# Performance work log

Hardware: AMD Instinct MI355X
Metric: run time of the kernel (lower is better)

## Reference

```python
import jax, jax.numpy as jnp
import numpy as np

B, D, W, T = 1024, 128, 512, 8
MAX_STEPS = 48
RTOL, ATOL = 1e-3, 1e-6
SAFETY, FMIN, FMAX = 0.9, 0.2, 10.0

# Tsit5 (Tsitouras 5(4)) tableau
A21 = 0.161
A31, A32 = -0.008480655492356989, 0.335480655492357
A41, A42, A43 = 2.8971530571054935, -6.359448489975075, 4.3622954328695815
A51, A52, A53, A54 = 5.325864828439257, -11.748883564062828, 7.4955393428898365, -0.09249506636175525
A61, A62, A63, A64, A65 = 5.86145544294642, -12.92096931784711, 8.159367898576159, -0.071584973281401, -0.028269050394068383
B1, B2, B3, B4, B5, B6 = 0.09646076681806523, 0.01, 0.4798896504144996, 1.379008574103742, -3.290069515436081, 2.324710524099774
E1, E2, E3, E4, E5, E6, E7 = (-0.00178001105222577714, -0.0008164344596567469, 0.007880878010261995,
                              -0.1447110071732629, 0.5823571654525552, -0.45808210592918697,
                              0.015151515151515152)


def setup_inputs() -> dict:
    key = jax.random.key(0)
    ks = jax.random.split(key, 9)
    def lin(k, fan_in, fan_out):
        s = 1.0 / np.sqrt(fan_in)
        return jax.random.normal(k, (fan_out, fan_in), jnp.float32) * s
    ts = jnp.linspace(0.0, 1.0, T, dtype=jnp.float32)
    y0 = jax.random.normal(ks[0], (B, D), jnp.float32)
    return {
        "ts": ts, "y0": y0,
        "W0": lin(ks[1], D, W), "b0": jnp.zeros((W,), jnp.float32),
        "W1": lin(ks[2], W, W), "b1": jnp.zeros((W,), jnp.float32),
        "W2": lin(ks[3], W, D), "b2": jnp.zeros((D,), jnp.float32),
    }


def _solve(ts, y0, W0, b0, W1, b1, W2, b2):
    def f(y):  # MLP vector field: D -> W -> W -> D, softplus activations
        h = jax.nn.softplus(y @ W0.T + b0)
        h = jax.nn.softplus(h @ W1.T + b1)
        return h @ W2.T + b2

    nT = ts.shape[0]
    ys0 = jnp.zeros((nT,) + y0.shape, y0.dtype).at[0].set(y0)  # SaveAt includes t0
    carry0 = (ts[0], ts[1] - ts[0], y0, jnp.int32(1), ys0)

    def step(carry, _):
        t, dt, y, si, ys = carry
        done = si >= nT
        si_c = jnp.minimum(si, nT - 1)
        tns = ts[si_c]
        # clip step to next save time (one shared dt across batch: unvmap_dt=True)
        h = jnp.where(done, 0.0, jnp.maximum(jnp.minimum(dt, tns - t), 0.0))
        k1 = f(y)
        k2 = f(y + h * (A21 * k1))
        k3 = f(y + h * (A31 * k1 + A32 * k2))
        k4 = f(y + h * (A41 * k1 + A42 * k2 + A43 * k3))
        k5 = f(y + h * (A51 * k1 + A52 * k2 + A53 * k3 + A54 * k4))
        k6 = f(y + h * (A61 * k1 + A62 * k2 + A63 * k3 + A64 * k4 + A65 * k5))
        y_new = y + h * (B1 * k1 + B2 * k2 + B3 * k3 + B4 * k4 + B5 * k5 + B6 * k6)
        k7 = f(y_new)
        err = h * (E1 * k1 + E2 * k2 + E3 * k3 + E4 * k4 + E5 * k5 + E6 * k6 + E7 * k7)
        scale = ATOL + RTOL * jnp.maximum(jnp.abs(y), jnp.abs(y_new))
        enorm = jnp.sqrt(jnp.mean((err / scale) ** 2))  # global norm -> shared dt
        accept = (enorm <= 1.0) & (~done)
        t_new = t + h
        hit = accept & (t_new >= tns - 1e-6)
        y = jnp.where(accept, y_new, y)
        t = jnp.where(accept, t_new, t)
        cur = jax.lax.dynamic_index_in_dim(ys, si_c, 0, keepdims=False)
        ys = jax.lax.dynamic_update_index_in_dim(ys, jnp.where(hit, y, cur), si_c, 0)
        si = si + hit.astype(si.dtype)
        safe_e = jnp.where(enorm > 0.0, enorm, 1.0)
        factor = jnp.where(enorm > 0.0, jnp.clip(SAFETY * safe_e ** (-0.2), FMIN, FMAX), FMAX)
        dt = jnp.where(done, dt, dt * factor)
        return (t, dt, y, si, ys), None

    (_, _, _, _, ys), _ = jax.lax.scan(step, carry0, None, length=MAX_STEPS)
    return ys  # [T, B, D]


def reference(ts, y0, W0, b0, W1, b1, W2, b2):
    return _solve(ts, y0, W0, b0, W1, b1, W2, b2)
```

## Files before the change

### kernel.cpp

```cpp
#include <hip/hip_runtime.h>
#include <math.h>

#define DEVFN static __device__ __forceinline__

constexpr int Bn = 1024, Dn = 128, Wn = 512, Tn = 8;
constexpr int NSTEP = 48;
constexpr int RPB = 4;
constexpr int NBLK = Bn / RPB;
constexpr int NTHR = 1024;
constexpr int BD = Bn * Dn;

constexpr size_t OFF_SLOTS = 0;
constexpr size_t OFF_STATE = 512;
constexpr size_t OFF_W0T   = 1024;
constexpr size_t OFF_W1T   = OFF_W0T + (size_t)Dn*Wn*4;
constexpr size_t OFF_W2T   = OFF_W1T + (size_t)Wn*Wn*4;
constexpr size_t OFF_Y     = OFF_W2T + (size_t)Wn*Dn*4;
constexpr size_t OFF_K     = OFF_Y   + (size_t)2*BD*4;

struct OdeState { int si; int cur; float t; float dt; };

constexpr float A21f = 0.161f;
constexpr float A31f = -0.008480655492356989f, A32f = 0.335480655492357f;
constexpr float A41f = 2.8971530571054935f, A42f = -6.359448489975075f, A43f = 4.3622954328695815f;
constexpr float A51f = 5.325864828439257f, A52f = -11.748883564062828f, A53f = 7.4955393428898365f, A54f = -0.09249506636175525f;
constexpr float A61f = 5.86145544294642f, A62f = -12.92096931784711f, A63f = 8.159367898576159f, A64f = -0.071584973281401f, A65f = -0.028269050394068383f;
constexpr float B1f = 0.09646076681806523f, B2f = 0.01f, B3f = 0.4798896504144996f, B4f = 1.379008574103742f, B5f = -3.290069515436081f, B6f = 2.324710524099774f;
constexpr float E1f = -0.00178001105222577714f, E2f = -0.0008164344596567469f, E3f = 0.007880878010261995f, E4f = -0.1447110071732629f, E5f = 0.5823571654525552f, E6f = -0.45808210592918697f, E7f = 0.015151515151515152f;

DEVFN float softplusf(float x) {
  return fmaxf(x, 0.f) + log1pf(expf(-fabsf(x)));
}

template<int K, int O, bool ACT, bool GOUT>
DEVFN void dense_layer(const float* __restrict__ zl, const float* __restrict__ WT,
                       const float* __restrict__ bias, float* __restrict__ pl,
                       float* __restrict__ outl, float* __restrict__ outg, int tid)
{
  constexpr int CG   = O / 4;
  constexpr int KSPL = NTHR / CG;
  constexpr int KL   = K / KSPL;
  static_assert(CG * KSPL == NTHR, "mapping");
  static_assert(KSPL * KL == K, "ksplit");

  const int kg = tid / CG;
  const int cg = tid % CG;
  const int oc = cg * 4;
  const int i0 = kg * KL;

  float acc[4][4];
#pragma unroll
  for (int r = 0; r < 4; ++r)
#pragma unroll
    for (int c = 0; c < 4; ++c) acc[r][c] = 0.f;

#pragma unroll 2
  for (int i = i0; i < i0 + KL; i += 4) {
    float zv[4][4];
#pragma unroll
    for (int r = 0; r < 4; ++r) {
      const float4 zt = *(const float4*)&zl[r*K + i];
      zv[r][0] = zt.x; zv[r][1] = zt.y; zv[r][2] = zt.z; zv[r][3] = zt.w;
    }
#pragma unroll
    for (int ii = 0; ii < 4; ++ii) {
      const float4 w = *(const float4*)&WT[(size_t)(i + ii)*O + oc];
#pragma unroll
      for (int r = 0; r < 4; ++r) {
        acc[r][0] = fmaf(zv[r][ii], w.x, acc[r][0]);
        acc[r][1] = fmaf(zv[r][ii], w.y, acc[r][1]);
        acc[r][2] = fmaf(zv[r][ii], w.z, acc[r][2]);
        acc[r][3] = fmaf(zv[r][ii], w.w, acc[r][3]);
      }
    }
  }
#pragma unroll
  for (int r = 0; r < 4; ++r) {
    float4 v; v.x = acc[r][0]; v.y = acc[r][1]; v.z = acc[r][2]; v.w = acc[r][3];
    *(float4*)&pl[(size_t)(kg*4 + r)*O + oc] = v;
  }
  __syncthreads();
  for (int e = tid; e < 4*O; e += NTHR) {
    const int r = e / O, c = e % O;
    float s = 0.f;
#pragma unroll
    for (int k2 = 0; k2 < KSPL; ++k2) s += pl[(size_t)(k2*4 + r)*O + c];
    s += bias[c];
    if (ACT) s = softplusf(s);
    outl[r*O + c] = s;
    if (GOUT) outg[e] = s;
  }
  __syncthreads();
}

DEVFN void eval_f(const float* __restrict__ zl, float* __restrict__ h1l,
                  float* __restrict__ h2l, float* __restrict__ pl,
                  float* __restrict__ kout, float* __restrict__ kglob,
                  const float* __restrict__ W0T, const float* __restrict__ W1T,
                  const float* __restrict__ W2T,
                  const float* __restrict__ b0, const float* __restrict__ b1,
                  const float* __restrict__ b2, int tid)
{
  dense_layer<Dn, Wn, true,  false>(zl,  W0T, b0, pl, h1l, nullptr, tid);
  dense_layer<Wn, Wn, true,  false>(h1l, W1T, b1, pl, h2l, nullptr, tid);
  if (kglob) dense_layer<Wn, Dn, false, true >(h2l, W2T, b2, pl, kout, kglob, tid);
  else       dense_layer<Wn, Dn, false, false>(h2l, W2T, b2, pl, kout, nullptr, tid);
}

template<int N>
DEVFN void combine(float* __restrict__ zl, const float* __restrict__ yl, float h,
                   const float* c, const float (*kkl)[RPB*Dn],
                   float* __restrict__ yglob, int tid)
{
  for (int e = tid; e < RPB*Dn; e += NTHR) {
    float a = c[0] * kkl[0][e];
#pragma unroll
    for (int l = 1; l < N; ++l) a = fmaf(c[l], kkl[l][e], a);
    const float v = fmaf(h, a, yl[e]);
    zl[e] = v;
    if (yglob) yglob[e] = v;
  }
}

__global__ __launch_bounds__(256) void ode_init(
    const float* __restrict__ ts, const float* __restrict__ y0,
    const float* __restrict__ W0, const float* __restrict__ W1,
    const float* __restrict__ W2, char* __restrict__ ws, float* __restrict__ out)
{
  const int idx = blockIdx.x * blockDim.x + threadIdx.x;
  float* W0T = (float*)(ws + OFF_W0T);
  float* W1T = (float*)(ws + OFF_W1T);
  float* W2T = (float*)(ws + OFF_W2T);
  float* y0b = (float*)(ws + OFF_Y);
  double* slots = (double*)(ws + OFF_SLOTS);

  if (idx < Tn*BD) out[idx] = (idx < BD) ? y0[idx] : 0.f;
  if (idx < BD) y0b[idx] = y0[idx];
  if (idx < Dn*Wn) { const int i = idx >> 9, o = idx & (Wn-1); W0T[idx] = W0[o*Dn + i]; }
  if (idx < Wn*Wn) { const int i = idx >> 9, o = idx & (Wn-1); W1T[idx] = W1[o*Wn + i]; }
  if (idx < Wn*Dn) { const int i = idx >> 7, o = idx & (Dn-1); W2T[idx] = W2[o*Wn + i]; }
  if (idx < NSTEP) slots[idx] = 0.0;
  if (idx == 0) {
    OdeState s0; s0.si = 1; s0.cur = 0; s0.t = 0.f; s0.dt = ts[1] - ts[0];
    *(OdeState*)(ws + OFF_STATE)      = s0;
    *(OdeState*)(ws + OFF_STATE + 64) = s0;
  }
}

__global__ __launch_bounds__(NTHR) void ode_step(
    int s, const float* __restrict__ ts,
    const float* __restrict__ b0, const float* __restrict__ b1,
    const float* __restrict__ b2,
    char* __restrict__ ws, float* __restrict__ out)
{
  const float* W0T = (const float*)(ws + OFF_W0T);
  const float* W1T = (const float*)(ws + OFF_W1T);
  const float* W2T = (const float*)(ws + OFF_W2T);
  float* ybuf = (float*)(ws + OFF_Y);
  float* kbuf = (float*)(ws + OFF_K);
  double* slots = (double*)(ws + OFF_SLOTS);

  __shared__ __align__(16) float zl[RPB*Dn];
  __shared__ __align__(16) float yl[RPB*Dn];
  __shared__ __align__(16) float h1l[RPB*Wn];
  __shared__ __align__(16) float h2l[RPB*Wn];
  __shared__ __align__(16) float pl[16384];
  __shared__ __align__(16) float kkl[7][RPB*Dn];
  __shared__ float wred[NTHR/64];

  const int tid  = threadIdx.x;
  const int row0 = blockIdx.x * RPB;

  OdeState st = *(const OdeState*)(ws + OFF_STATE + 64*(s & 1));

  if (s > 0) {
    const bool donep = st.si >= Tn;
    const int sic = min(st.si, Tn - 1);
    const float tns = ts[sic];
    const float h = donep ? 0.f : fmaxf(fminf(st.dt, tns - st.t), 0.f);
    const float enorm = (float)sqrt(slots[s-1] / (double)BD);
    const bool accept = (enorm <= 1.f) && !donep;
    const float tnew = st.t + h;
    const bool hit = accept && (tnew >= tns - 1e-6f);
    if (accept) { st.cur ^= 1; st.t = tnew; }
    if (hit) {
      const float* yn = ybuf + (size_t)st.cur*BD + row0*Dn;
      float* op = out + (size_t)sic*BD + row0*Dn;
      for (int e = tid; e < RPB*Dn; e += NTHR) op[e] = yn[e];
      st.si += 1;
    }
    if (!donep) {
      const float safe_e = (enorm > 0.f) ? enorm : 1.f;
      const float factor = (enorm > 0.f)
          ? fminf(fmaxf(0.9f * powf(safe_e, -0.2f), 0.2f), 10.f) : 10.f;
      st.dt *= factor;
    }
    if (blockIdx.x == 0 && tid == 0)
      *(OdeState*)(ws + OFF_STATE + 64*((s+1) & 1)) = st;
  }

  if (st.si >= Tn || s >= NSTEP) return;

  const int sic = min(st.si, Tn - 1);
  const float tns = ts[sic];
  const float h = fmaxf(fminf(st.dt, tns - st.t), 0.f);

  const float* yg = ybuf + (size_t)st.cur*BD + row0*Dn;
  for (int e = tid; e < RPB*Dn; e += NTHR) yl[e] = yg[e];

  if (s == 0) {
    for (int e = tid; e < RPB*Dn; e += NTHR) zl[e] = yg[e];
    __syncthreads();
    eval_f(zl, h1l, h2l, pl, kkl[0], kbuf + (size_t)st.cur*BD + row0*Dn,
           W0T, W1T, W2T, b0, b1, b2, tid);
  } else {
    const float* kg = kbuf + (size_t)st.cur*BD + row0*Dn;
    for (int e = tid; e < RPB*Dn; e += NTHR) kkl[0][e] = kg[e];
    __syncthreads();
  }

  { const float c[1] = {A21f};
    combine<1>(zl, yl, h, c, kkl, nullptr, tid); }
  __syncthreads();
  eval_f(zl, h1l, h2l, pl, kkl[1], nullptr, W0T, W1T, W2T, b0, b1, b2, tid);

  { const float c[2] = {A31f, A32f};
    combine<2>(zl, yl, h, c, kkl, nullptr, tid); }
  __syncthreads();
  eval_f(zl, h1l, h2l, pl, kkl[2], nullptr, W0T, W1T, W2T, b0, b1, b2, tid);

  { const float c[3] = {A41f, A42f, A43f};
    combine<3>(zl, yl, h, c, kkl, nullptr, tid); }
  __syncthreads();
  eval_f(zl, h1l, h2l, pl, kkl[3], nullptr, W0T, W1T, W2T, b0, b1, b2, tid);

  { const float c[4] = {A51f, A52f, A53f, A54f};
    combine<4>(zl, yl, h, c, kkl, nullptr, tid); }
  __syncthreads();
  eval_f(zl, h1l, h2l, pl, kkl[4], nullptr, W0T, W1T, W2T, b0, b1, b2, tid);

  { const float c[5] = {A61f, A62f, A63f, A64f, A65f};
    combine<5>(zl, yl, h, c, kkl, nullptr, tid); }
  __syncthreads();
  eval_f(zl, h1l, h2l, pl, kkl[5], nullptr, W0T, W1T, W2T, b0, b1, b2, tid);

  { const float c[6] = {B1f, B2f, B3f, B4f, B5f, B6f};
    combine<6>(zl, yl, h, c, kkl, ybuf + (size_t)(st.cur^1)*BD + row0*Dn, tid); }
  __syncthreads();
  eval_f(zl, h1l, h2l, pl, kkl[6], kbuf + (size_t)(st.cur^1)*BD + row0*Dn,
         W0T, W1T, W2T, b0, b1, b2, tid);

  float local = 0.f;
  for (int e = tid; e < RPB*Dn; e += NTHR) {
    float a = E1f * kkl[0][e];
    a = fmaf(E2f, kkl[1][e], a);
    a = fmaf(E3f, kkl[2][e], a);
    a = fmaf(E4f, kkl[3][e], a);
    a = fmaf(E5f, kkl[4][e], a);
    a = fmaf(E6f, kkl[5][e], a);
    a = fmaf(E7f, kkl[6][e], a);
    const float ev = h * a;
    const float sc = fmaf(1e-3f, fmaxf(fabsf(yl[e]), fabsf(zl[e])), 1e-6f);
    const float q = ev / sc;
    local = fmaf(q, q, local);
  }
#pragma unroll
  for (int off = 32; off > 0; off >>= 1) local += __shfl_down(local, off);
  if ((tid & 63) == 0) wred[tid >> 6] = local;
  __syncthreads();
  if (tid == 0) {
    float tot = 0.f;
#pragma unroll
    for (int w = 0; w < NTHR/64; ++w) tot += wred[w];
    atomicAdd(&slots[s], (double)tot);
  }
}

extern "C" void kernel_launch(void* const* d_in, const int* in_sizes, int n_in,
                              void* d_out, int out_size, void* d_ws, size_t ws_size,
                              hipStream_t stream) {
  (void)in_sizes; (void)n_in; (void)out_size; (void)ws_size;
  const float* ts = (const float*)d_in[0];
  const float* y0 = (const float*)d_in[1];
  const float* W0 = (const float*)d_in[2];
  const float* b0 = (const float*)d_in[3];
  const float* W1 = (const float*)d_in[4];
  const float* b1 = (const float*)d_in[5];
  const float* W2 = (const float*)d_in[6];
  const float* b2 = (const float*)d_in[7];
  float* out = (float*)d_out;
  char* ws = (char*)d_ws;

  hipLaunchKernelGGL(ode_init, dim3((Tn*BD)/256), dim3(256), 0, stream,
                     ts, y0, W0, W1, W2, ws, out);
  for (int s = 0; s <= NSTEP; ++s)
    hipLaunchKernelGGL(ode_step, dim3(NBLK), dim3(NTHR), 0, stream,
                       s, ts, b0, b1, b2, ws, out);
}
```

Baseline: 940.9 us.

## Fuse per-step launches into persistent cooperative kernel with grid sync

Replaces the 49 per-step kernel launches with a single cooperative persistent kernel. State, y and k7 stay in shared memory and registers across steps, and blocks synchronise on the global error norm with grid.sync. The dense layer now reduces its K-split partial sums with wave shuffles instead of a large shared-memory scratch buffer and an extra barrier, and biases are staged in shared memory. This removes launch overhead, the global round trips of y and k, and the shared partial-sum buffer, at the cost of a grid-wide barrier each step and requiring all 256 blocks of 1024 threads to be co-resident.

Result: slower. 1.388 ms (+47.5%).

```diff
diff --git a/kernel.cpp b/kernel.cpp
--- a/kernel.cpp
+++ b/kernel.cpp
@@ -1,5 +1,8 @@
 #include <hip/hip_runtime.h>
+#include <hip/hip_cooperative_groups.h>
 #include <math.h>
+
+namespace cg = cooperative_groups;
 
 #define DEVFN static __device__ __forceinline__
 
@@ -11,14 +14,9 @@
 constexpr int BD = Bn * Dn;
 
 constexpr size_t OFF_SLOTS = 0;
-constexpr size_t OFF_STATE = 512;
 constexpr size_t OFF_W0T   = 1024;
 constexpr size_t OFF_W1T   = OFF_W0T + (size_t)Dn*Wn*4;
 constexpr size_t OFF_W2T   = OFF_W1T + (size_t)Wn*Wn*4;
-constexpr size_t OFF_Y     = OFF_W2T + (size_t)Wn*Dn*4;
-constexpr size_t OFF_K     = OFF_Y   + (size_t)2*BD*4;
-
-struct OdeState { int si; int cur; float t; float dt; };
 
 constexpr float A21f = 0.161f;
 constexpr float A31f = -0.008480655492356989f, A32f = 0.335480655492357f;
@@ -32,21 +30,25 @@
   return fmaxf(x, 0.f) + log1pf(expf(-fabsf(x)));
 }
 
-template<int K, int O, bool ACT, bool GOUT>
+template<int K, int O, bool ACT>
 DEVFN void dense_layer(const float* __restrict__ zl, const float* __restrict__ WT,
-                       const float* __restrict__ bias, float* __restrict__ pl,
-                       float* __restrict__ outl, float* __restrict__ outg, int tid)
+                       const float* __restrict__ biasl, float* __restrict__ outl,
+                       int tid)
 {
   constexpr int CG   = O / 4;
   constexpr int KSPL = NTHR / CG;
   constexpr int KL   = K / KSPL;
+  constexpr int CGW  = 64 / KSPL;
   static_assert(CG * KSPL == NTHR, "mapping");
   static_assert(KSPL * KL == K, "ksplit");
-
-  const int kg = tid / CG;
-  const int cg = tid % CG;
-  const int oc = cg * 4;
-  const int i0 = kg * KL;
+  static_assert(CGW * KSPL == 64, "wave");
+
+  const int lane = tid & 63;
+  const int wid  = tid >> 6;
+  const int cgl  = lane & (CGW - 1);
+  const int kg   = lane / CGW;
+  const int oc   = (wid * CGW + cgl) * 4;
+  const int i0   = kg * KL;
 
   float acc[4][4];
 #pragma unroll
@@ -54,76 +56,70 @@
 #pragma unroll
     for (int c = 0; c < 4; ++c) acc[r][c] = 0.f;
 
+  const float* wp = WT + i0 * O + oc;
+  const float* zp = zl + i0;
+
+#define ROWFMA(r, zs, wv) \
+  acc[r][0] = fmaf(zs, wv.x, acc[r][0]); \
+  acc[r][1] = fmaf(zs, wv.y, acc[r][1]); \
+  acc[r][2] = fmaf(zs, wv.z, acc[r][2]); \
+  acc[r][3] = fmaf(zs, wv.w, acc[r][3]);
+#define IIFMA(wv, comp) ROWFMA(0, z0.comp, wv) ROWFMA(1, z1.comp, wv) \
+                        ROWFMA(2, z2.comp, wv) ROWFMA(3, z3.comp, wv)
+
 #pragma unroll 2
-  for (int i = i0; i < i0 + KL; i += 4) {
-    float zv[4][4];
-#pragma unroll
-    for (int r = 0; r < 4; ++r) {
-      const float4 zt = *(const float4*)&zl[r*K + i];
-      zv[r][0] = zt.x; zv[r][1] = zt.y; zv[r][2] = zt.z; zv[r][3] = zt.w;
-    }
-#pragma unroll
-    for (int ii = 0; ii < 4; ++ii) {
-      const float4 w = *(const float4*)&WT[(size_t)(i + ii)*O + oc];
-#pragma unroll
-      for (int r = 0; r < 4; ++r) {
-        acc[r][0] = fmaf(zv[r][ii], w.x, acc[r][0]);
-        acc[r][1] = fmaf(zv[r][ii], w.y, acc[r][1]);
-        acc[r][2] = fmaf(zv[r][ii], w.z, acc[r][2]);
-        acc[r][3] = fmaf(zv[r][ii], w.w, acc[r][3]);
-      }
-    }
-  }
-#pragma unroll
-  for (int r = 0; r < 4; ++r) {
-    float4 v; v.x = acc[r][0]; v.y = acc[r][1]; v.z = acc[r][2]; v.w = acc[r][3];
-    *(float4*)&pl[(size_t)(kg*4 + r)*O + oc] = v;
-  }
-  __syncthreads();
-  for (int e = tid; e < 4*O; e += NTHR) {
-    const int r = e / O, c = e % O;
-    float s = 0.f;
-#pragma unroll
-    for (int k2 = 0; k2 < KSPL; ++k2) s += pl[(size_t)(k2*4 + r)*O + c];
-    s += bias[c];
-    if (ACT) s = softplusf(s);
-    outl[r*O + c] = s;
-    if (GOUT) outg[e] = s;
-  }
-  __syncthreads();
-}
-
-DEVFN void eval_f(const float* __restrict__ zl, float* __restrict__ h1l,
-                  float* __restrict__ h2l, float* __restrict__ pl,
-                  float* __restrict__ kout, float* __restrict__ kglob,
-                  const float* __restrict__ W0T, const float* __restrict__ W1T,
-                  const float* __restrict__ W2T,
-                  const float* __restrict__ b0, const float* __restrict__ b1,
-                  const float* __restrict__ b2, int tid)
-{
-  dense_layer<Dn, Wn, true,  false>(zl,  W0T, b0, pl, h1l, nullptr, tid);
-  dense_layer<Wn, Wn, true,  false>(h1l, W1T, b1, pl, h2l, nullptr, tid);
-  if (kglob) dense_layer<Wn, Dn, false, true >(h2l, W2T, b2, pl, kout, kglob, tid);
-  else       dense_layer<Wn, Dn, false, false>(h2l, W2T, b2, pl, kout, nullptr, tid);
+  for (int i = 0; i < KL; i += 4) {
+    const float4 z0 = *(const float4*)&zp[0*K + i];
+    const float4 z1 = *(const float4*)&zp[1*K + i];
+    const float4 z2 = *(const float4*)&zp[2*K + i];
+    const float4 z3 = *(const float4*)&zp[3*K + i];
+    const float4 wa = *(const float4*)&wp[0];
+    const float4 wb = *(const float4*)&wp[O];
+    const float4 wc = *(const float4*)&wp[2*O];
+    const float4 wd = *(const float4*)&wp[3*O];
+    IIFMA(wa, x) IIFMA(wb, y) IIFMA(wc, z) IIFMA(wd, w)
+    wp += 4 * O;
+  }
+#undef IIFMA
+#undef ROWFMA
+
+#pragma unroll
+  for (int m = CGW; m < 64; m <<= 1) {
+#pragma unroll
+    for (int r = 0; r < 4; ++r)
+#pragma unroll
+      for (int c = 0; c < 4; ++c)
+        acc[r][c] += __shfl_xor(acc[r][c], m, 64);
+  }
+
+  if (kg < 4) {
+    const int r = kg;
+    const float4 b4 = *(const float4*)&biasl[oc];
+    float4 v;
+    v.x = acc[r][0] + b4.x; v.y = acc[r][1] + b4.y;
+    v.z = acc[r][2] + b4.z; v.w = acc[r][3] + b4.w;
+    if (ACT) {
+      v.x = softplusf(v.x); v.y = softplusf(v.y);
+      v.z = softplusf(v.z); v.w = softplusf(v.w);
+    }
+    *(float4*)&outl[r*O + oc] = v;
+  }
 }
 
 template<int N>
 DEVFN void combine(float* __restrict__ zl, const float* __restrict__ yl, float h,
-                   const float* c, const float (*kkl)[RPB*Dn],
-                   float* __restrict__ yglob, int tid)
+                   const float* c, const float (*kkl)[RPB*Dn], int tid)
 {
   for (int e = tid; e < RPB*Dn; e += NTHR) {
     float a = c[0] * kkl[0][e];
 #pragma unroll
     for (int l = 1; l < N; ++l) a = fmaf(c[l], kkl[l][e], a);
-    const float v = fmaf(h, a, yl[e]);
-    zl[e] = v;
-    if (yglob) yglob[e] = v;
+    zl[e] = fmaf(h, a, yl[e]);
   }
 }
 
 __global__ __launch_bounds__(256) void ode_init(
-    const float* __restrict__ ts, const float* __restrict__ y0,
+    const float* __restrict__ y0,
     const float* __restrict__ W0, const float* __restrict__ W1,
     const float* __restrict__ W2, char* __restrict__ ws, float* __restrict__ out)
 {
@@ -131,24 +127,17 @@
   float* W0T = (float*)(ws + OFF_W0T);
   float* W1T = (float*)(ws + OFF_W1T);
   float* W2T = (float*)(ws + OFF_W2T);
-  float* y0b = (float*)(ws + OFF_Y);
   double* slots = (double*)(ws + OFF_SLOTS);
 
   if (idx < Tn*BD) out[idx] = (idx < BD) ? y0[idx] : 0.f;
-  if (idx < BD) y0b[idx] = y0[idx];
   if (idx < Dn*Wn) { const int i = idx >> 9, o = idx & (Wn-1); W0T[idx] = W0[o*Dn + i]; }
   if (idx < Wn*Wn) { const int i = idx >> 9, o = idx & (Wn-1); W1T[idx] = W1[o*Wn + i]; }
   if (idx < Wn*Dn) { const int i = idx >> 7, o = idx & (Dn-1); W2T[idx] = W2[o*Wn + i]; }
   if (idx < NSTEP) slots[idx] = 0.0;
-  if (idx == 0) {
-    OdeState s0; s0.si = 1; s0.cur = 0; s0.t = 0.f; s0.dt = ts[1] - ts[0];
-    *(OdeState*)(ws + OFF_STATE)      = s0;
-    *(OdeState*)(ws + OFF_STATE + 64) = s0;
-  }
-}
-
-__global__ __launch_bounds__(NTHR) void ode_step(
-    int s, const float* __restrict__ ts,
+}
+
+__global__ __launch_bounds__(NTHR, 4) void ode_persist(
+    const float* __restrict__ ts, const float* __restrict__ y0,
     const float* __restrict__ b0, const float* __restrict__ b1,
     const float* __restrict__ b2,
     char* __restrict__ ws, float* __restrict__ out)
@@ -156,123 +145,122 @@
   const float* W0T = (const float*)(ws + OFF_W0T);
   const float* W1T = (const float*)(ws + OFF_W1T);
   const float* W2T = (const float*)(ws + OFF_W2T);
-  float* ybuf = (float*)(ws + OFF_Y);
-  float* kbuf = (float*)(ws + OFF_K);
   double* slots = (double*)(ws + OFF_SLOTS);
 
+  __shared__ __align__(16) float yl[RPB*Dn];
   __shared__ __align__(16) float zl[RPB*Dn];
-  __shared__ __align__(16) float yl[RPB*Dn];
   __shared__ __align__(16) float h1l[RPB*Wn];
   __shared__ __align__(16) float h2l[RPB*Wn];
-  __shared__ __align__(16) float pl[16384];
   __shared__ __align__(16) float kkl[7][RPB*Dn];
+  __shared__ __align__(16) float b0l[Wn], b1l[Wn], b2l[Dn];
+  __shared__ float tsl[Tn];
   __shared__ float wred[NTHR/64];
+  __shared__ double ered;
 
   const int tid  = threadIdx.x;
   const int row0 = blockIdx.x * RPB;
-
-  OdeState st = *(const OdeState*)(ws + OFF_STATE + 64*(s & 1));
-
-  if (s > 0) {
-    const bool donep = st.si >= Tn;
-    const int sic = min(st.si, Tn - 1);
-    const float tns = ts[sic];
-    const float h = donep ? 0.f : fmaxf(fminf(st.dt, tns - st.t), 0.f);
-    const float enorm = (float)sqrt(slots[s-1] / (double)BD);
-    const bool accept = (enorm <= 1.f) && !donep;
-    const float tnew = st.t + h;
+  cg::grid_group grid = cg::this_grid();
+
+  for (int e = tid; e < Wn; e += NTHR) { b0l[e] = b0[e]; b1l[e] = b1[e]; }
+  for (int e = tid; e < Dn; e += NTHR) b2l[e] = b2[e];
+  if (tid < Tn) tsl[tid] = ts[tid];
+  {
+    const float* yg = y0 + row0*Dn;
+    for (int e = tid; e < RPB*Dn; e += NTHR) { const float v = yg[e]; yl[e] = v; zl[e] = v; }
+  }
+  __syncthreads();
+
+  dense_layer<Dn, Wn, true >(zl,  W0T, b0l, h1l, tid); __syncthreads();
+  dense_layer<Wn, Wn, true >(h1l, W1T, b1l, h2l, tid); __syncthreads();
+  dense_layer<Wn, Dn, false>(h2l, W2T, b2l, kkl[0], tid); __syncthreads();
+
+  int   si = 1;
+  float t  = 0.f;
+  float dt = tsl[1] - tsl[0];
+
+  for (int s = 0; s < NSTEP; ++s) {
+    if (si >= Tn) break;
+    const int sic = (si < Tn-1) ? si : Tn-1;
+    const float tns = tsl[sic];
+    const float h = fmaxf(fminf(dt, tns - t), 0.f);
+
+#define EVALF(dst) \
+    dense_layer<Dn, Wn, true >(zl,  W0T, b0l, h1l, tid); __syncthreads(); \
+    dense_layer<Wn, Wn, true >(h1l, W1T, b1l, h2l, tid); __syncthreads(); \
+    dense_layer<Wn, Dn, false>(h2l, W2T, b2l, dst, tid); __syncthreads();
+
+    { const float c[1] = {A21f};
+      combine<1>(zl, yl, h, c, kkl, tid); } __syncthreads();
+    EVALF(kkl[1])
+    { const float c[2] = {A31f, A32f};
+      combine<2>(zl, yl, h, c, kkl, tid); } __syncthreads();
+    EVALF(kkl[2])
+    { const float c[3] = {A41f, A42f, A43f};
+      combine<3>(zl, yl, h, c, kkl, tid); } __syncthreads();
+    EVALF(kkl[3])
+    { const float c[4] = {A51f, A52f, A53f, A54f};
+      combine<4>(zl, yl, h, c, kkl, tid); } __syncthreads();
+    EVALF(kkl[4])
+    { const float c[5] = {A61f, A62f, A63f, A64f, A65f};
+      combine<5>(zl, yl, h, c, kkl, tid); } __syncthreads();
+    EVALF(kkl[5])
+    { const float c[6] = {B1f, B2f, B3f, B4f, B5f, B6f};
+      combine<6>(zl, yl, h, c, kkl, tid); } __syncthreads();
+    EVALF(kkl[6])
+#undef EVALF
+
+    float local = 0.f;
+    for (int e = tid; e < RPB*Dn; e += NTHR) {
+      float a = E1f * kkl[0][e];
+      a = fmaf(E2f, kkl[1][e], a);
+      a = fmaf(E3f, kkl[2][e], a);
+      a = fmaf(E4f, kkl[3][e], a);
+      a = fmaf(E5f, kkl[4][e], a);
+      a = fmaf(E6f, kkl[5][e], a);
+      a = fmaf(E7f, kkl[6][e], a);
+      const float ev = h * a;
+      const float sc = fmaf(1e-3f, fmaxf(fabsf(yl[e]), fabsf(zl[e])), 1e-6f);
+      const float q = ev / sc;
+      local = fmaf(q, q, local);
+    }
+#pragma unroll
+    for (int off = 32; off > 0; off >>= 1) local += __shfl_down(local, off);
+    if ((tid & 63) == 0) wred[tid >> 6] = local;
+    __syncthreads();
+    if (tid == 0) {
+      float tot = 0.f;
+#pragma unroll
+      for (int w = 0; w < NTHR/64; ++w) tot += wred[w];
+      atomicAdd(&slots[s], (double)tot);
+    }
+
+    grid.sync();
+
+    if (tid == 0)
+      ered = __hip_atomic_load(&slots[s], __ATOMIC_RELAXED, __HIP_MEMORY_SCOPE_AGENT);
+    __syncthreads();
+
+    const float enorm = (float)sqrt(ered / (double)BD);
+    const bool accept = (enorm <= 1.f);
+    const float tnew = t + h;
     const bool hit = accept && (tnew >= tns - 1e-6f);
-    if (accept) { st.cur ^= 1; st.t = tnew; }
-    if (hit) {
-      const float* yn = ybuf + (size_t)st.cur*BD + row0*Dn;
-      float* op = out + (size_t)sic*BD + row0*Dn;
-      for (int e = tid; e < RPB*Dn; e += NTHR) op[e] = yn[e];
-      st.si += 1;
-    }
-    if (!donep) {
+
+    if (accept) {
+      t = tnew;
+      for (int e = tid; e < RPB*Dn; e += NTHR) { yl[e] = zl[e]; kkl[0][e] = kkl[6][e]; }
+      if (hit) {
+        float* op = out + (size_t)sic*BD + row0*Dn;
+        for (int e = tid; e < RPB*Dn; e += NTHR) op[e] = zl[e];
+        si += 1;
+      }
+    }
+    {
       const float safe_e = (enorm > 0.f) ? enorm : 1.f;
       const float factor = (enorm > 0.f)
           ? fminf(fmaxf(0.9f * powf(safe_e, -0.2f), 0.2f), 10.f) : 10.f;
-      st.dt *= factor;
-    }
-    if (blockIdx.x == 0 && tid == 0)
-      *(OdeState*)(ws + OFF_STATE + 64*((s+1) & 1)) = st;
-  }
-
-  if (st.si >= Tn || s >= NSTEP) return;
-
-  const int sic = min(st.si, Tn - 1);
-  const float tns = ts[sic];
-  const float h = fmaxf(fminf(st.dt, tns - st.t), 0.f);
-
-  const float* yg = ybuf + (size_t)st.cur*BD + row0*Dn;
-  for (int e = tid; e < RPB*Dn; e += NTHR) yl[e] = yg[e];
-
-  if (s == 0) {
-    for (int e = tid; e < RPB*Dn; e += NTHR) zl[e] = yg[e];
+      dt *= factor;
+    }
     __syncthreads();
-    eval_f(zl, h1l, h2l, pl, kkl[0], kbuf + (size_t)st.cur*BD + row0*Dn,
-           W0T, W1T, W2T, b0, b1, b2, tid);
-  } else {
-    const float* kg = kbuf + (size_t)st.cur*BD + row0*Dn;
-    for (int e = tid; e < RPB*Dn; e += NTHR) kkl[0][e] = kg[e];
-    __syncthreads();
-  }
-
-  { const float c[1] = {A21f};
-    combine<1>(zl, yl, h, c, kkl, nullptr, tid); }
-  __syncthreads();
-  eval_f(zl, h1l, h2l, pl, kkl[1], nullptr, W0T, W1T, W2T, b0, b1, b2, tid);
-
-  { const float c[2] = {A31f, A32f};
-    combine<2>(zl, yl, h, c, kkl, nullptr, tid); }
-  __syncthreads();
-  eval_f(zl, h1l, h2l, pl, kkl[2], nullptr, W0T, W1T, W2T, b0, b1, b2, tid);
-
-  { const float c[3] = {A41f, A42f, A43f};
-    combine<3>(zl, yl, h, c, kkl, nullptr, tid); }
-  __syncthreads();
-  eval_f(zl, h1l, h2l, pl, kkl[3], nullptr, W0T, W1T, W2T, b0, b1, b2, tid);
-
-  { const float c[4] = {A51f, A52f, A53f, A54f};
-    combine<4>(zl, yl, h, c, kkl, nullptr, tid); }
-  __syncthreads();
-  eval_f(zl, h1l, h2l, pl, kkl[4], nullptr, W0T, W1T, W2T, b0, b1, b2, tid);
-
-  { const float c[5] = {A61f, A62f, A63f, A64f, A65f};
-    combine<5>(zl, yl, h, c, kkl, nullptr, tid); }
-  __syncthreads();
-  eval_f(zl, h1l, h2l, pl, kkl[5], nullptr, W0T, W1T, W2T, b0, b1, b2, tid);
-
-  { const float c[6] = {B1f, B2f, B3f, B4f, B5f, B6f};
-    combine<6>(zl, yl, h, c, kkl, ybuf + (size_t)(st.cur^1)*BD + row0*Dn, tid); }
-  __syncthreads();
-  eval_f(zl, h1l, h2l, pl, kkl[6], kbuf + (size_t)(st.cur^1)*BD + row0*Dn,
-         W0T, W1T, W2T, b0, b1, b2, tid);
-
-  float local = 0.f;
-  for (int e = tid; e < RPB*Dn; e += NTHR) {
-    float a = E1f * kkl[0][e];
-    a = fmaf(E2f, kkl[1][e], a);
-    a = fmaf(E3f, kkl[2][e], a);
-    a = fmaf(E4f, kkl[3][e], a);
-    a = fmaf(E5f, kkl[4][e], a);
-    a = fmaf(E6f, kkl[5][e], a);
-    a = fmaf(E7f, kkl[6][e], a);
-    const float ev = h * a;
-    const float sc = fmaf(1e-3f, fmaxf(fabsf(yl[e]), fabsf(zl[e])), 1e-6f);
-    const float q = ev / sc;
-    local = fmaf(q, q, local);
-  }
-#pragma unroll
-  for (int off = 32; off > 0; off >>= 1) local += __shfl_down(local, off);
-  if ((tid & 63) == 0) wred[tid >> 6] = local;
-  __syncthreads();
-  if (tid == 0) {
-    float tot = 0.f;
-#pragma unroll
-    for (int w = 0; w < NTHR/64; ++w) tot += wred[w];
-    atomicAdd(&slots[s], (double)tot);
   }
 }
 
@@ -292,8 +280,10 @@
   char* ws = (char*)d_ws;
 
   hipLaunchKernelGGL(ode_init, dim3((Tn*BD)/256), dim3(256), 0, stream,
-                     ts, y0, W0, W1, W2, ws, out);
-  for (int s = 0; s <= NSTEP; ++s)
-    hipLaunchKernelGGL(ode_step, dim3(NBLK), dim3(NTHR), 0, stream,
-                       s, ts, b0, b1, b2, ws, out);
-}
+                     y0, W0, W1, W2, ws, out);
+
+  void* args[] = { (void*)&ts, (void*)&y0, (void*)&b0, (void*)&b1,
+                   (void*)&b2, (void*)&ws, (void*)&out };
+  (void)hipLaunchCooperativeKernel((const void*)ode_persist, dim3(NBLK), dim3(NTHR),
+                                   args, 0, stream);
+}
```
